# Optimization experiments

Hardware: AMD Instinct MI355X
Metric: run time of the kernel (lower is better)

## Reference

```python
import jax, jax.numpy as jnp
import numpy as np

BN_INV = 1.0 / np.float32(np.sqrt(1.0 + 1e-5))  # eval BN with running_mean=0, running_var=1


def _conv(x, w, stride):
    return jax.lax.conv_general_dilated(
        x, w, (stride, stride), [(1, 1), (1, 1)],
        dimension_numbers=('NCHW', 'OIHW', 'NCHW'))


def _se(x, w1, b1, w2, b2):
    # squeeze-excite: global avg pool -> fc -> relu -> fc -> sigmoid -> scale
    y = x.mean(axis=(2, 3))                       # (B, C)
    y = jax.nn.relu(y @ w1.T + b1)
    y = jax.nn.sigmoid(y @ w2.T + b2)
    return x * y[:, :, None, None]


def _squash(s):
    n2 = jnp.sum(s * s, axis=-1, keepdims=True)
    n = jnp.sqrt(n2)
    return s * (n2 / (1.0 + n2)) / (n + 1e-8)


def _block(x, cw, g, b, s1w, s1b, s2w, s2b, stride):
    h = _conv(x, cw, stride)
    h = h * (g * BN_INV)[None, :, None, None] + b[None, :, None, None]
    h = jax.nn.relu(h)
    return _se(h, s1w, s1b, s2w, s2b)


def setup_inputs() -> dict:
    key = jax.random.key(0)
    ks = jax.random.split(key, 32)
    rn = lambda i, shape, s=1.0: s * jax.random.normal(ks[i], shape, dtype=jnp.float32)
    d = {}
    d['x'] = rn(0, (64, 1, 128, 128))
    # feature extractor
    d['conv1_w'] = rn(1, (16, 1, 3, 3), 0.3)
    d['bn1_g'] = 1.0 + rn(2, (16,), 0.1)
    d['bn1_b'] = rn(3, (16,), 0.1)
    d['se1_w1'] = rn(4, (1, 16), 0.2); d['se1_b1'] = rn(5, (1,), 0.1)
    d['se1_w2'] = rn(6, (16, 1), 0.2); d['se1_b2'] = rn(7, (16,), 0.1)
    d['conv2_w'] = rn(8, (32, 16, 3, 3), 0.1)
    d['bn2_g'] = 1.0 + rn(9, (32,), 0.1)
    d['bn2_b'] = rn(10, (32,), 0.1)
    d['se2_w1'] = rn(11, (2, 32), 0.2); d['se2_b1'] = rn(12, (2,), 0.1)
    d['se2_w2'] = rn(13, (32, 2), 0.2); d['se2_b2'] = rn(14, (32,), 0.1)
    d['conv3_w'] = rn(15, (64, 32, 3, 3), 0.07)
    d['bn3_g'] = 1.0 + rn(16, (64,), 0.1)
    d['bn3_b'] = rn(17, (64,), 0.1)
    d['se3_w1'] = rn(18, (4, 64), 0.15); d['se3_b1'] = rn(19, (4,), 0.1)
    d['se3_w2'] = rn(20, (64, 4), 0.15); d['se3_b2'] = rn(21, (64,), 0.1)
    # primary capsules conv: 64 -> 8 caps * 8 dim = 64 channels, stride 2
    d['pc_w'] = rn(22, (64, 64, 3, 3), 0.05)
    d['pc_b'] = rn(23, (64,), 0.05)
    # digit capsule transform: (1, 2048, 3, 16, 8)
    d['W_digit'] = 0.01 * jax.random.normal(ks[24], (1, 2048, 3, 16, 8), dtype=jnp.float32)
    return d


def reference(x, conv1_w, bn1_g, bn1_b, se1_w1, se1_b1, se1_w2, se1_b2,
              conv2_w, bn2_g, bn2_b, se2_w1, se2_b1, se2_w2, se2_b2,
              conv3_w, bn3_g, bn3_b, se3_w1, se3_b1, se3_w2, se3_b2,
              pc_w, pc_b, W_digit):
    h = _block(x, conv1_w, bn1_g, bn1_b, se1_w1, se1_b1, se1_w2, se1_b2, 1)
    h = _block(h, conv2_w, bn2_g, bn2_b, se2_w1, se2_b1, se2_w2, se2_b2, 2)
    h = _block(h, conv3_w, bn3_g, bn3_b, se3_w1, se3_b1, se3_w2, se3_b2, 2)
    # primary capsules: conv -> (B, 8 caps, 8 dim, 16*16) -> (B, 2048, 8)
    u = _conv(h, pc_w, 2) + pc_b[None, :, None, None]     # (B, 64, 16, 16)
    B = u.shape[0]
    u = u.reshape(B, 8, 8, -1).transpose(0, 1, 3, 2).reshape(B, -1, 8)
    u = _squash(u)                                        # (B, 2048, 8)
    # u_hat[b,i,c,d] = sum_e W[0,i,c,d,e] * u[b,i,e]  (avoids torch's W.repeat)
    u_hat = jnp.einsum('icde,bie->bicd', W_digit[0], u)   # (B, 2048, 3, 16)
    b_ij = jnp.zeros((B, u_hat.shape[1], u_hat.shape[2], 1), u_hat.dtype)
    v_j = None
    for _ in range(3):  # fixed routing iterations
        c_ij = jax.nn.softmax(b_ij, axis=2)
        s_j = jnp.sum(c_ij * u_hat, axis=1, keepdims=True)  # (B,1,3,16)
        v_j = _squash(s_j)
        b_ij = b_ij + jnp.sum(u_hat * v_j, axis=-1, keepdims=True)
    v = v_j[:, 0]                                          # (B, 3, 16)
    return jnp.sqrt(jnp.sum(v * v, axis=-1))               # (B, 3) class lengths
```

## Files before the change

### kernel.cpp

```cpp
#include <hip/hip_runtime.h>
#include <math.h>

#define BN_INV_F 0.9999950000374997f

__device__ __forceinline__ void gload_lds4(const float* g, float* l) {
    __builtin_amdgcn_global_load_lds(
        (const __attribute__((address_space(1))) void*)g,
        (__attribute__((address_space(3))) void*)l, 4, 0, 0);
}

__global__ __launch_bounds__(256) void wtrans_all_k(
    const float* __restrict__ w1, const float* __restrict__ w2,
    const float* __restrict__ w3, const float* __restrict__ wp,
    float* __restrict__ w1t, float* __restrict__ w2t,
    float* __restrict__ w3t, float* __restrict__ wpt)
{
    int i = blockIdx.x * 256 + threadIdx.x;
    if (i < 144) {
        int co = i % 16, k = i / 16;
        w1t[i] = w1[co * 9 + k];
    } else if (i < 4752) {
        int t = i - 144;
        int co = t % 32, rk = t / 32, cin = rk / 9, k = rk % 9;
        w2t[t] = w2[(co * 16 + cin) * 9 + k];
    } else if (i < 23184) {
        int t = i - 4752;
        int co = t % 64, rk = t / 64, cin = rk / 9, k = rk % 9;
        w3t[t] = w3[(co * 32 + cin) * 9 + k];
    } else if (i < 60048) {
        int t = i - 23184;
        int co = t % 64, rk = t / 64, cin = rk / 9, k = rk % 9;
        wpt[t] = wp[(co * 64 + cin) * 9 + k];
    }
}

template <int CIN, int CINB, int COUT, int COB, int HIN, int HOUT, int STRIDE,
          int TW, int ROWS_T, int PPT, int CB, int NTHREADS,
          bool BN_RELU, bool SE_SUM, int HSE_IN, int KSPLIT>
__global__ __launch_bounds__(NTHREADS) void convt_k(
    const float* __restrict__ in, const float* __restrict__ wt,
    const float* __restrict__ gamma,
    const float* __restrict__ beta,
    float* __restrict__ out, size_t pstride,
    float* __restrict__ se_sum,
    const float* __restrict__ se_sums_in,
    const float* __restrict__ se_w1, const float* __restrict__ se_b1,
    const float* __restrict__ se_w2, const float* __restrict__ se_b2,
    float inv_spatial)
{
    constexpr int WIN = HIN, WOUT = HOUT;
    constexpr int TH = ROWS_T * PPT;
    constexpr int IH_T = (TH - 1) * STRIDE + 3;
    constexpr int NW = NTHREADS / 64;
    constexpr int NCHUNK = CINB / CB;
    constexpr int SEGS = (WIN >= 64) ? (WIN / 64) : 1;
    constexpr int PAIRS = (IH_T + 1) / 2;
    constexpr int NG = COUT / COB;
    static_assert(NTHREADS == TW * ROWS_T, "geometry");
    static_assert(TW == WOUT, "tile must span full output width");
    static_assert(CINB % CB == 0, "chunking");
    static_assert(WIN % 64 == 0 || WIN == 32, "stage width");

    const int b = blockIdx.z;
    const int gy = blockIdx.y;
    const int ty = blockIdx.x;
    const int tid = threadIdx.x;
    const int wo = tid % TW;
    const int rg = tid / TW;
    const int g = gy % NG;
    const int kk = gy / NG;
    const int cin0 = kk * CINB;

    __shared__ float in_t[2][CB * IH_T * WIN];
    __shared__ float scl[CIN];
    __shared__ float gl[COB], bl[COB];
    __shared__ float red[NW][COB];
    __shared__ float hid[HSE_IN > 0 ? HSE_IN : 1];

    const float* inb = in + (size_t)b * CIN * HIN * WIN;
    const int gr0 = ty * TH * STRIDE - 1;
    const int wos = wo * STRIDE;
    const int wvid = tid >> 6, lane = tid & 63;

    auto stage = [&](int c, int buf) {
        const int cb0 = cin0 + c * CB;
        float* bb = &in_t[buf][0];
        if (WIN >= 64) {
            for (int r = wvid; r < CB * IH_T; r += NW) {
                int ci = r / IH_T, lr = r - ci * IH_T;
                int gr = gr0 + lr;
                float* ldst = bb + (ci * IH_T + lr) * WIN;
                if (gr >= 0 && gr < HIN) {
                    const float* gsrc = inb + (size_t)(cb0 + ci) * HIN * WIN + (size_t)gr * WIN;
#pragma unroll
                    for (int s = 0; s < SEGS; ++s)
                        gload_lds4(gsrc + s * 64 + lane, ldst + s * 64);
                } else {
#pragma unroll
                    for (int s = 0; s < SEGS; ++s) ldst[s * 64 + lane] = 0.0f;
                }
            }
        } else {
            for (int pz = wvid; pz < CB * PAIRS; pz += NW) {
                int ci = pz / PAIRS, q = pz - ci * PAIRS;
                int lr0 = q * 2;
                int nr = (lr0 + 1 < IH_T) ? 2 : 1;
                int grr = gr0 + lr0;
                float* ldst = bb + (ci * IH_T + lr0) * WIN;
                if (nr == 2 && grr >= 0 && grr + 1 < HIN) {
                    const float* gsrc = inb + (size_t)(cb0 + ci) * HIN * WIN + (size_t)grr * WIN + lane;
                    gload_lds4(gsrc, ldst);
                } else {
                    for (int e = lane; e < nr * WIN; e += 64) {
                        int rr = e / WIN, cc = e - rr * WIN;
                        int gr = grr + rr;
                        ldst[e] = (gr >= 0 && gr < HIN)
                            ? inb[(size_t)(cb0 + ci) * HIN * WIN + (size_t)gr * WIN + cc] : 0.0f;
                    }
                }
            }
        }
    };

    stage(0, 0);

    if (HSE_IN > 0) {
        if (tid < HSE_IN) {
            float a = se_b1[tid];
            for (int c = 0; c < CIN; ++c)
                a = fmaf(se_sums_in[b * CIN + c] * inv_spatial, se_w1[tid * CIN + c], a);
            hid[tid] = fmaxf(a, 0.0f);
        }
        __syncthreads();
        if (tid < CIN) {
            float a = se_b2[tid];
            for (int h = 0; h < HSE_IN; ++h)
                a = fmaf(hid[h], se_w2[tid * HSE_IN + h], a);
            scl[tid] = 1.0f / (1.0f + expf(-a));
        }
    } else {
        for (int t = tid; t < CIN; t += NTHREADS) scl[t] = 1.0f;
    }
    if (tid < COB) {
        int co = g * COB + tid;
        if (BN_RELU) {
            gl[tid] = gamma[co] * BN_INV_F;
            bl[tid] = beta[co];
        } else {
            gl[tid] = (kk == 0) ? gamma[co] : 0.0f;
        }
    }

    float acc[PPT][COB];
#pragma unroll
    for (int p = 0; p < PPT; ++p)
#pragma unroll
        for (int co = 0; co < COB; ++co) acc[p][co] = 0.0f;

    int cur = 0;
    for (int c = 0; c < NCHUNK; ++c) {
        asm volatile("s_waitcnt vmcnt(0)" ::: "memory");
        __syncthreads();
        if (c + 1 < NCHUNK) stage(c + 1, cur ^ 1);

        const float* bb = &in_t[cur][0];
        for (int ci = 0; ci < CB; ++ci) {
            const int cw = cin0 + c * CB + ci;
            const float sc = scl[cw];
            const float* wtap = wt + (size_t)cw * 9 * COUT + g * COB;
#pragma unroll
            for (int kh = 0; kh < 3; ++kh) {
#pragma unroll
                for (int kw = 0; kw < 3; ++kw) {
                    const float* wrow = wtap + (kh * 3 + kw) * COUT;
#pragma unroll
                    for (int p = 0; p < PPT; ++p) {
                        const float* row = bb + (ci * IH_T + (rg + p * ROWS_T) * STRIDE + kh) * WIN;
                        int wi = wos + kw - 1;
                        float v;
                        if (kw == 0) {
                            v = row[wi < 0 ? 0 : wi];
                            if (wi < 0) v = 0.0f;
                        } else if (STRIDE == 1 && kw == 2) {
                            v = row[wi >= WIN ? WIN - 1 : wi];
                            if (wi >= WIN) v = 0.0f;
                        } else {
                            v = row[wi];
                        }
                        v *= sc;
#pragma unroll
                        for (int co = 0; co < COB; ++co)
                            acc[p][co] = fmaf(wrow[co], v, acc[p][co]);
                    }
                }
            }
        }
        cur ^= 1;
    }

    float tsum[COB];
#pragma unroll
    for (int co = 0; co < COB; ++co) tsum[co] = 0.0f;
    float* ob = out + (size_t)kk * pstride
              + ((size_t)b * COUT + (size_t)g * COB) * HOUT * WOUT;
#pragma unroll
    for (int p = 0; p < PPT; ++p) {
        const int ho = ty * TH + rg + p * ROWS_T;
#pragma unroll
        for (int co = 0; co < COB; ++co) {
            float v;
            if (BN_RELU)
                v = fmaxf(fmaf(acc[p][co], gl[co], bl[co]), 0.0f);
            else
                v = acc[p][co] + gl[co];
            ob[(size_t)co * HOUT * WOUT + ho * WOUT + wo] = v;
            tsum[co] += v;
        }
    }

    if (SE_SUM) {
#pragma unroll
        for (int co = 0; co < COB; ++co) {
            float v = tsum[co];
            for (int off = 32; off; off >>= 1) v += __shfl_down(v, off, 64);
            if (lane == 0) red[wvid][co] = v;
        }
        __syncthreads();
        if (tid < COB) {
            float v = 0.0f;
#pragma unroll
            for (int k = 0; k < NW; ++k) v += red[k][tid];
            atomicAdd(&se_sum[b * COUT + g * COB + tid], v);
        }
    }
}

__global__ __launch_bounds__(256) void squash4_k(const float* __restrict__ up,
                                                 size_t pstride,
                                                 float* __restrict__ u)
{
    const int idx = blockIdx.x * 256 + threadIdx.x;
    const int b = idx >> 11, i = idx & 2047;
    const int chi = i >> 8, spx = i & 255;
    const size_t off = ((size_t)(b * 64 + chi * 8)) * 256 + spx;
    float s[8];
    float n2 = 0.0f;
#pragma unroll
    for (int j = 0; j < 8; j++) {
        const size_t o = off + (size_t)j * 256;
        s[j] = (up[o] + up[o + pstride]) + (up[o + 2 * pstride] + up[o + 3 * pstride]);
        n2 = fmaf(s[j], s[j], n2);
    }
    const float n = sqrtf(n2);
    const float f = (n2 / (1.0f + n2)) / (n + 1e-8f);
    float* q = u + (size_t)idx * 8;
#pragma unroll
    for (int j = 0; j < 8; j++) q[j] = s[j] * f;
}

__global__ __launch_bounds__(256) void uhat_k(const float* __restrict__ u,
                                              const float* __restrict__ W,
                                              float* __restrict__ u_hat)
{
    const int idx = blockIdx.x * 256 + threadIdx.x;
    const int cd = idx % 48;
    const int bi = idx / 48;
    const int i = bi & 2047;
    const float* uu = u + (size_t)bi * 8;
    const float* wp = W + (size_t)i * 384 + cd * 8;
    float a = 0.0f;
#pragma unroll
    for (int e = 0; e < 8; e++) a = fmaf(wp[e], uu[e], a);
    u_hat[idx] = a;
}

template <int IT>
__global__ __launch_bounds__(256) void sweep_k(const float* __restrict__ u_hat,
                                               const float* __restrict__ s_hist,
                                               float* __restrict__ s_out)
{
    const int b = blockIdx.y;
    const int i = blockIdx.x * 256 + threadIdx.x;
    const int tid = threadIdx.x;
    __shared__ float vsh[IT > 0 ? IT : 1][48];
    __shared__ float fac[IT > 0 ? IT : 1][3];
    __shared__ float red[4][48];

    const float4* qp = (const float4*)(u_hat + ((size_t)b * 2048 + i) * 48);
    float uhv[48];
#pragma unroll
    for (int q = 0; q < 12; ++q) {
        float4 t = qp[q];
        uhv[q * 4 + 0] = t.x; uhv[q * 4 + 1] = t.y;
        uhv[q * 4 + 2] = t.z; uhv[q * 4 + 3] = t.w;
    }

    if (IT > 0) {
        if (tid < IT * 48) {
            int t = tid / 48, c = tid % 48;
            vsh[t][c] = s_hist[((size_t)t * 64 + b) * 48 + c];
        }
        __syncthreads();
        if (tid < IT * 3) {
            int t = tid / 3, j = tid % 3;
            float n2 = 0.0f;
            for (int d = 0; d < 16; ++d) { float s = vsh[t][j * 16 + d]; n2 = fmaf(s, s, n2); }
            float n = sqrtf(n2);
            fac[t][j] = (n2 / (1.0f + n2)) / (n + 1e-8f);
        }
        __syncthreads();
        if (tid < IT * 48) {
            int t = tid / 48, c = tid % 48;
            vsh[t][c] *= fac[t][c / 16];
        }
        __syncthreads();
    }

    float c0, c1, c2;
    if (IT == 0) {
        c0 = c1 = c2 = (1.0f / 3.0f);
    } else {
        float b0 = 0.0f, b1 = 0.0f, b2 = 0.0f;
#pragma unroll
        for (int t = 0; t < IT; ++t)
#pragma unroll
            for (int d = 0; d < 16; ++d) {
                b0 = fmaf(uhv[d],      vsh[t][d],      b0);
                b1 = fmaf(uhv[16 + d], vsh[t][16 + d], b1);
                b2 = fmaf(uhv[32 + d], vsh[t][32 + d], b2);
            }
        float m = fmaxf(b0, fmaxf(b1, b2));
        float e0 = expf(b0 - m), e1 = expf(b1 - m), e2 = expf(b2 - m);
        float inv = 1.0f / (e0 + e1 + e2);
        c0 = e0 * inv; c1 = e1 * inv; c2 = e2 * inv;
    }

    float sp[48];
#pragma unroll
    for (int d = 0; d < 16; ++d) {
        sp[d]      = c0 * uhv[d];
        sp[16 + d] = c1 * uhv[16 + d];
        sp[32 + d] = c2 * uhv[32 + d];
    }
    const int lane = tid & 63, wv = tid >> 6;
#pragma unroll
    for (int j = 0; j < 48; ++j) {
        float x = sp[j];
        for (int off = 32; off; off >>= 1) x += __shfl_down(x, off, 64);
        if (lane == 0) red[wv][j] = x;
    }
    __syncthreads();
    if (tid < 48) {
        float x = red[0][tid] + red[1][tid] + red[2][tid] + red[3][tid];
        atomicAdd(&s_out[(size_t)b * 48 + tid], x);
    }
}

__global__ __launch_bounds__(64) void route_out_k(const float* __restrict__ s2,
                                                  float* __restrict__ out)
{
    const int b = blockIdx.x;
    __shared__ float s[48];
    if (threadIdx.x < 48) s[threadIdx.x] = s2[(size_t)b * 48 + threadIdx.x];
    __syncthreads();
    if (threadIdx.x < 3) {
        int j = threadIdx.x;
        float n2 = 0.0f;
        for (int d = 0; d < 16; ++d) { float v = s[j * 16 + d]; n2 = fmaf(v, v, n2); }
        float n = sqrtf(n2);
        float fc = (n2 / (1.0f + n2)) / (n + 1e-8f);
        out[b * 3 + j] = fc * n;
    }
}

extern "C" void kernel_launch(void* const* d_in, const int* in_sizes, int n_in,
                              void* d_out, int out_size, void* d_ws, size_t ws_size,
                              hipStream_t stream)
{
    const float* x       = (const float*)d_in[0];
    const float* conv1_w = (const float*)d_in[1];
    const float* bn1_g   = (const float*)d_in[2];
    const float* bn1_b   = (const float*)d_in[3];
    const float* se1_w1  = (const float*)d_in[4];
    const float* se1_b1  = (const float*)d_in[5];
    const float* se1_w2  = (const float*)d_in[6];
    const float* se1_b2  = (const float*)d_in[7];
    const float* conv2_w = (const float*)d_in[8];
    const float* bn2_g   = (const float*)d_in[9];
    const float* bn2_b   = (const float*)d_in[10];
    const float* se2_w1  = (const float*)d_in[11];
    const float* se2_b1  = (const float*)d_in[12];
    const float* se2_w2  = (const float*)d_in[13];
    const float* se2_b2  = (const float*)d_in[14];
    const float* conv3_w = (const float*)d_in[15];
    const float* bn3_g   = (const float*)d_in[16];
    const float* bn3_b   = (const float*)d_in[17];
    const float* se3_w1  = (const float*)d_in[18];
    const float* se3_b1  = (const float*)d_in[19];
    const float* se3_w2  = (const float*)d_in[20];
    const float* se3_b2  = (const float*)d_in[21];
    const float* pc_w    = (const float*)d_in[22];
    const float* pc_b    = (const float*)d_in[23];
    const float* W_digit = (const float*)d_in[24];

    float* ws = (float*)d_ws;
    float* h1     = ws;
    float* h2     = ws + 16777216;
    float* h3     = ws;
    float* uparts = ws + 4194304;
    float* u      = ws + 8388608;
    float* u_hat  = ws + 9437184;
    float* sums   = ws + 25165824;
    float* s1 = sums, *s2 = sums + 1024, *s3 = sums + 3072;
    float* s_buf  = sums + 7168;
    float* w1t    = ws + 25182208;
    float* w2t    = w1t + 144;
    float* w3t    = w2t + 4608;
    float* wpt    = w3t + 18432;

    hipMemsetAsync(sums, 0, 16384 * sizeof(float), stream);
    wtrans_all_k<<<235, 256, 0, stream>>>(conv1_w, conv2_w, conv3_w, pc_w,
                                          w1t, w2t, w3t, wpt);

    convt_k<1, 1, 16, 16, 128, 128, 1, 128, 2, 2, 1, 256, true, true, 0, 1>
        <<<dim3(32, 1, 64), 256, 0, stream>>>(
            x, w1t, bn1_g, bn1_b, h1, 0, s1,
            nullptr, nullptr, nullptr, nullptr, nullptr, 0.0f);

    convt_k<16, 16, 32, 32, 128, 64, 2, 64, 4, 1, 2, 256, true, true, 1, 1>
        <<<dim3(16, 1, 64), 256, 0, stream>>>(
            h1, w2t, bn2_g, bn2_b, h2, 0, s2,
            s1, se1_w1, se1_b1, se1_w2, se1_b2, 1.0f / 16384.0f);

    convt_k<32, 32, 64, 16, 64, 32, 2, 32, 8, 1, 2, 256, true, true, 2, 1>
        <<<dim3(4, 4, 64), 256, 0, stream>>>(
            h2, w3t, bn3_g, bn3_b, h3, 0, s3,
            s2, se2_w1, se2_b1, se2_w2, se2_b2, 1.0f / 4096.0f);

    convt_k<64, 16, 64, 16, 32, 16, 2, 16, 16, 1, 2, 256, false, false, 4, 4>
        <<<dim3(1, 16, 64), 256, 0, stream>>>(
            h3, wpt, pc_b, nullptr, uparts, (size_t)1048576, nullptr,
            s3, se3_w1, se3_b1, se3_w2, se3_b2, 1.0f / 1024.0f);

    squash4_k<<<512, 256, 0, stream>>>(uparts, (size_t)1048576, u);
    uhat_k<<<24576, 256, 0, stream>>>(u, W_digit, u_hat);

    sweep_k<0><<<dim3(8, 64), 256, 0, stream>>>(u_hat, s_buf, s_buf + 0 * 64 * 48);
    sweep_k<1><<<dim3(8, 64), 256, 0, stream>>>(u_hat, s_buf, s_buf + 1 * 64 * 48);
    sweep_k<2><<<dim3(8, 64), 256, 0, stream>>>(u_hat, s_buf, s_buf + 2 * 64 * 48);
    route_out_k<<<64, 64, 0, stream>>>(s_buf + 2 * 64 * 48, (float*)d_out);
}
```

Measured before the change: 236.1 us.

## Split conv3 over input channels with a separate combine, BN and SE-sum kernel

Conv3 now splits its 32 input channels into two halves, each writing a partial sum with a zero bias and no BN or SE reduction. A new combine kernel adds the two partials, applies BN and ReLU, writes h3, and computes the per-channel SE sums without atomics. The aim is more parallelism and shorter per-block reduction loops in conv3. An unrelated template parameter also changes from 2 to 4 in conv2, conv3 and the primary-capsule conv. The cost is an extra launch and an extra round trip of partial buffers through global memory.

```diff
diff --git a/kernel.cpp b/kernel.cpp
--- a/kernel.cpp
+++ b/kernel.cpp
@@ -233,6 +233,35 @@
             atomicAdd(&se_sum[b * COUT + g * COB + tid], v);
         }
     }
+}
+
+__global__ __launch_bounds__(256) void cb_k(const float* __restrict__ pA,
+                                            const float* __restrict__ pB,
+                                            const float* __restrict__ gamma,
+                                            const float* __restrict__ beta,
+                                            float* __restrict__ h3,
+                                            float* __restrict__ s3)
+{
+    const int bc = blockIdx.x;
+    const int c = bc & 63;
+    const int tid = threadIdx.x;
+    __shared__ float red[4];
+    const size_t base = (size_t)bc * 1024;
+    float4 a = ((const float4*)(pA + base))[tid];
+    float4 d = ((const float4*)(pB + base))[tid];
+    const float g = gamma[c] * BN_INV_F, be = beta[c];
+    float4 v;
+    v.x = fmaxf(fmaf(a.x + d.x, g, be), 0.0f);
+    v.y = fmaxf(fmaf(a.y + d.y, g, be), 0.0f);
+    v.z = fmaxf(fmaf(a.z + d.z, g, be), 0.0f);
+    v.w = fmaxf(fmaf(a.w + d.w, g, be), 0.0f);
+    ((float4*)(h3 + base))[tid] = v;
+    float s = (v.x + v.y) + (v.z + v.w);
+    for (int off = 32; off; off >>= 1) s += __shfl_down(s, off, 64);
+    const int lane = tid & 63, wv = tid >> 6;
+    if (lane == 0) red[wv] = s;
+    __syncthreads();
+    if (tid == 0) s3[bc] = (red[0] + red[1]) + (red[2] + red[3]);
 }
 
 __global__ __launch_bounds__(256) void squash4_k(const float* __restrict__ up,
@@ -407,18 +436,21 @@
     float* h1     = ws;
     float* h2     = ws + 16777216;
     float* h3     = ws;
+    float* cp0    = ws + 4194304;
+    float* cp1    = ws + 8388608;
     float* uparts = ws + 4194304;
     float* u      = ws + 8388608;
     float* u_hat  = ws + 9437184;
     float* sums   = ws + 25165824;
     float* s1 = sums, *s2 = sums + 1024, *s3 = sums + 3072;
     float* s_buf  = sums + 7168;
-    float* w1t    = ws + 25182208;
+    float* zeros64 = sums + 16384;
+    float* w1t    = ws + 25182272;
     float* w2t    = w1t + 144;
     float* w3t    = w2t + 4608;
     float* wpt    = w3t + 18432;
 
-    hipMemsetAsync(sums, 0, 16384 * sizeof(float), stream);
+    hipMemsetAsync(sums, 0, 16448 * sizeof(float), stream);
     wtrans_all_k<<<235, 256, 0, stream>>>(conv1_w, conv2_w, conv3_w, pc_w,
                                           w1t, w2t, w3t, wpt);
 
@@ -427,17 +459,19 @@
             x, w1t, bn1_g, bn1_b, h1, 0, s1,
             nullptr, nullptr, nullptr, nullptr, nullptr, 0.0f);
 
-    convt_k<16, 16, 32, 32, 128, 64, 2, 64, 4, 1, 2, 256, true, true, 1, 1>
+    convt_k<16, 16, 32, 32, 128, 64, 2, 64, 4, 1, 4, 256, true, true, 1, 1>
         <<<dim3(16, 1, 64), 256, 0, stream>>>(
             h1, w2t, bn2_g, bn2_b, h2, 0, s2,
             s1, se1_w1, se1_b1, se1_w2, se1_b2, 1.0f / 16384.0f);
 
-    convt_k<32, 32, 64, 16, 64, 32, 2, 32, 8, 1, 2, 256, true, true, 2, 1>
+    convt_k<32, 16, 64, 32, 64, 32, 2, 32, 8, 1, 4, 256, false, false, 2, 2>
         <<<dim3(4, 4, 64), 256, 0, stream>>>(
-            h2, w3t, bn3_g, bn3_b, h3, 0, s3,
+            h2, w3t, zeros64, nullptr, cp0, (size_t)4194304, nullptr,
             s2, se2_w1, se2_b1, se2_w2, se2_b2, 1.0f / 4096.0f);
 
-    convt_k<64, 16, 64, 16, 32, 16, 2, 16, 16, 1, 2, 256, false, false, 4, 4>
+    cb_k<<<4096, 256, 0, stream>>>(cp0, cp1, bn3_g, bn3_b, h3, s3);
+
+    convt_k<64, 16, 64, 16, 32, 16, 2, 16, 16, 1, 4, 256, false, false, 4, 4>
         <<<dim3(1, 16, 64), 256, 0, stream>>>(
             h3, wpt, pc_b, nullptr, uparts, (size_t)1048576, nullptr,
             s3, se3_w1, se3_b1, se3_w2, se3_b2, 1.0f / 1024.0f);
```

New measurement: 228.7 us. 3.2% less time.
